# Performance work log

Measured on AMD Instinct MI355X. Metric: run time of the kernel, lower is better.

## Reference

```python
import jax, jax.numpy as jnp
import numpy as np

T, B, F = 160, 640, 40
HID, PROJ, LAYERS = 768, 256, 3


def lstm_proj_layer(x, Wk, b, Wp, reverse=False):
    # x: [T, B, in]; Wk: [in+PROJ, 4*HID]; b: [4*HID]; Wp: [HID, PROJ]
    nb = x.shape[1]
    c0 = jnp.zeros((nb, HID), x.dtype)
    h0 = jnp.zeros((nb, PROJ), x.dtype)

    def step(carry, xt):
        c, h = carry
        z = jnp.concatenate([xt, h], axis=-1) @ Wk + b
        i, j, f, o = jnp.split(z, 4, axis=-1)  # TF LSTMCell gate order i,j,f,o
        c = jax.nn.sigmoid(f + 1.0) * c + jax.nn.sigmoid(i) * jnp.tanh(j)  # forget_bias=1.0
        h = (jax.nn.sigmoid(o) * jnp.tanh(c)) @ Wp  # projection
        return (c, h), h

    _, ys = jax.lax.scan(step, (c0, h0), x, reverse=reverse)
    return ys  # [T, B, PROJ], time-aligned with input even when reverse=True


def _run_stack(x, params, reverse):
    for (Wk, b, Wp) in params:
        x = lstm_proj_layer(x, Wk, b, Wp, reverse=reverse)
    return x


def setup_inputs() -> dict:
    key = jax.random.key(0)
    keys = jax.random.split(key, 1 + 6 * LAYERS)
    inp = {"batch": jax.random.normal(keys[0], (T, B, F), dtype=jnp.float32)}
    ki = 1
    for d in ("fw", "bw"):
        for l in range(LAYERS):
            in_dim = F if l == 0 else PROJ
            inp[f"Wk_{d}{l}"] = jax.random.normal(keys[ki], (in_dim + PROJ, 4 * HID), dtype=jnp.float32) * 0.05
            inp[f"b_{d}{l}"] = jnp.zeros((4 * HID,), dtype=jnp.float32)
            inp[f"Wp_{d}{l}"] = jax.random.normal(keys[ki + 1], (HID, PROJ), dtype=jnp.float32) * 0.05
            ki += 2
    return inp


def reference(batch,
              Wk_fw0, b_fw0, Wp_fw0, Wk_fw1, b_fw1, Wp_fw1, Wk_fw2, b_fw2, Wp_fw2,
              Wk_bw0, b_bw0, Wp_bw0, Wk_bw1, b_bw1, Wp_bw1, Wk_bw2, b_bw2, Wp_bw2):
    fw_params = [(Wk_fw0, b_fw0, Wp_fw0), (Wk_fw1, b_fw1, Wp_fw1), (Wk_fw2, b_fw2, Wp_fw2)]
    bw_params = [(Wk_bw0, b_bw0, Wp_bw0), (Wk_bw1, b_bw1, Wp_bw1), (Wk_bw2, b_bw2, Wp_bw2)]
    out_fw = _run_stack(batch, fw_params, reverse=False)
    out_bw = _run_stack(batch, bw_params, reverse=True)
    outputs = jnp.concatenate([out_fw, out_bw], axis=2)  # [T, B, 2*PROJ]
    embedded = (outputs[0] + outputs[-1]) / 2.0
    # tf.nn.l2_normalize semantics
    embedded = embedded * jax.lax.rsqrt(jnp.maximum(jnp.sum(embedded * embedded, axis=-1, keepdims=True), 1e-12))
    return embedded
```

## Files before the change

### kernel.cpp

```cpp
#include <hip/hip_runtime.h>


typedef _Float16 h8 __attribute__((ext_vector_type(8)));
typedef float f4 __attribute__((ext_vector_type(4)));

#define T_STEPS 160
#define NB 640
#define HID 768
#define PROJ 256
#define NGATE 3072

__device__ __forceinline__ float sigm(float x) { return 1.0f / (1.0f + __expf(-x)); }
__device__ __forceinline__ float tanh_fast(float x) { return 2.0f / (1.0f + __expf(-2.0f * x)) - 1.0f; }

struct GateArgs {
  const _Float16* A0[6];
  const _Float16* A1[6];
  const _Float16* Bw[6];
  const float*    bias[6];
  float*          cst[6];
  _Float16*       g[6];
  int w0[6];
  int lda0[6];
  int K[6];
  int act[6];
};

struct ProjArgs {
  const _Float16* G[6];
  const _Float16* Wp[6];
  _Float16* out[6];
  _Float16* out2[6];
  int act[6];
};

__global__ __launch_bounds__(512) void gate_step(GateArgs args) {
  const int z = blockIdx.z;
  if (!args.act[z]) return;

  __shared__ __align__(16) char sm[36864];
  _Float16 (*As)[72] = (_Float16(*)[72])sm;
  _Float16 (*Bs)[72] = (_Float16(*)[72])(sm + 18432);
  float (*zs)[65] = (float(*)[65])sm;

  const _Float16* A0 = args.A0[z];
  const _Float16* A1 = args.A1[z];
  const _Float16* Bw = args.Bw[z];
  const int w0 = args.w0[z], lda0 = args.lda0[z], K = args.K[z];
  const int n0 = blockIdx.x * 128;
  const int m0 = blockIdx.y * 128;
  const int tid = threadIdx.x;
  const int lane = tid & 63;
  const int wv = tid >> 6;
  const int wm = (wv & 3) * 32;
  const int wn = (wv >> 2) * 64;

  f4 acc[2][4] = {};

  const int lr = tid >> 3;
  const int lkg = (tid & 7) * 8;

  for (int k0 = 0; k0 < K; k0 += 64) {
    const int gk = k0 + lkg;
    h8 av0, av1;
    if (gk < w0) {
      av0 = *(const h8*)(A0 + (size_t)(m0 + lr) * lda0 + gk);
      av1 = *(const h8*)(A0 + (size_t)(m0 + lr + 64) * lda0 + gk);
    } else {
      av0 = *(const h8*)(A1 + (size_t)(m0 + lr) * 256 + (gk - w0));
      av1 = *(const h8*)(A1 + (size_t)(m0 + lr + 64) * 256 + (gk - w0));
    }
    h8 bv0 = *(const h8*)(Bw + (size_t)(n0 + lr) * K + gk);
    h8 bv1 = *(const h8*)(Bw + (size_t)(n0 + lr + 64) * K + gk);
    __syncthreads();
    *(h8*)&As[lr][lkg] = av0;
    *(h8*)&As[lr + 64][lkg] = av1;
    *(h8*)&Bs[lr][lkg] = bv0;
    *(h8*)&Bs[lr + 64][lkg] = bv1;
    __syncthreads();
#pragma unroll
    for (int kk = 0; kk < 2; ++kk) {
      const int kq = ((lane >> 4) * 8) + kk * 32;
      h8 af[2], bf[4];
#pragma unroll
      for (int i = 0; i < 2; ++i)
        af[i] = *(const h8*)&As[wm + (lane & 15) + 16 * i][kq];
#pragma unroll
      for (int j = 0; j < 4; ++j)
        bf[j] = *(const h8*)&Bs[wn + (lane & 15) + 16 * j][kq];
#pragma unroll
      for (int i = 0; i < 2; ++i)
#pragma unroll
        for (int j = 0; j < 4; ++j)
          acc[i][j] = __builtin_amdgcn_mfma_f32_16x16x32_f16(af[i], bf[j], acc[i][j], 0, 0, 0);
    }
  }

  const float* bias = args.bias[z];
  float* cstate = args.cst[z];
  _Float16* gout = args.g[z];
#pragma unroll
  for (int p = 0; p < 2; ++p) {
    __syncthreads();
    if ((wv >> 2) == p) {
#pragma unroll
      for (int mi = 0; mi < 2; ++mi)
#pragma unroll
        for (int ni = 0; ni < 4; ++ni)
#pragma unroll
          for (int r = 0; r < 4; ++r) {
            int row = wm + mi * 16 + ((lane >> 4) << 2) + r;
            int col = ni * 16 + (lane & 15);
            zs[row][col] = acc[mi][ni][r];
          }
    }
    __syncthreads();
    const int u0 = (n0 + p * 64) >> 2;
#pragma unroll
    for (int it = 0; it < 4; ++it) {
      int item = it * 512 + tid;
      int row = item >> 4;
      int u = item & 15;
      float zi = zs[row][4 * u + 0] + bias[0 * HID + u0 + u];
      float zj = zs[row][4 * u + 1] + bias[1 * HID + u0 + u];
      float zf = zs[row][4 * u + 2] + bias[2 * HID + u0 + u];
      float zo = zs[row][4 * u + 3] + bias[3 * HID + u0 + u];
      size_t co = (size_t)(m0 + row) * HID + u0 + u;
      float cold = cstate[co];
      float cnew = sigm(zf + 1.0f) * cold + sigm(zi) * tanh_fast(zj);
      float g = sigm(zo) * tanh_fast(cnew);
      cstate[co] = cnew;
      gout[co] = (_Float16)g;
    }
  }
}

__global__ __launch_bounds__(256) void proj_step(ProjArgs args) {
  const int z = blockIdx.z;
  if (!args.act[z]) return;

  __shared__ __align__(16) _Float16 As[64][72];
  __shared__ __align__(16) _Float16 Bs[64][72];

  const _Float16* A = args.G[z];
  const _Float16* B = args.Wp[z];
  const int n0 = blockIdx.x * 64;
  const int m0 = blockIdx.y * 64;
  const int tid = threadIdx.x;
  const int lane = tid & 63;
  const int wv = tid >> 6;
  const int wm = (wv & 1) * 32;
  const int wn = (wv >> 1) * 32;

  f4 acc[2][2] = {};
  const int lr = tid >> 3;
  const int lkg = (tid & 7) * 8;

  for (int k0 = 0; k0 < HID; k0 += 64) {
    const int gk = k0 + lkg;
    h8 av0 = *(const h8*)(A + (size_t)(m0 + lr) * HID + gk);
    h8 av1 = *(const h8*)(A + (size_t)(m0 + lr + 32) * HID + gk);
    h8 bv0 = *(const h8*)(B + (size_t)(n0 + lr) * HID + gk);
    h8 bv1 = *(const h8*)(B + (size_t)(n0 + lr + 32) * HID + gk);
    __syncthreads();
    *(h8*)&As[lr][lkg] = av0;
    *(h8*)&As[lr + 32][lkg] = av1;
    *(h8*)&Bs[lr][lkg] = bv0;
    *(h8*)&Bs[lr + 32][lkg] = bv1;
    __syncthreads();
    const int mr = wm + (lane & 15);
    const int nr = wn + (lane & 15);
#pragma unroll
    for (int kk = 0; kk < 2; ++kk) {
      const int kq = ((lane >> 4) * 8) + kk * 32;
      h8 a0 = *(const h8*)&As[mr][kq];
      h8 a1 = *(const h8*)&As[mr + 16][kq];
      h8 b0 = *(const h8*)&Bs[nr][kq];
      h8 b1 = *(const h8*)&Bs[nr + 16][kq];
      acc[0][0] = __builtin_amdgcn_mfma_f32_16x16x32_f16(a0, b0, acc[0][0], 0, 0, 0);
      acc[0][1] = __builtin_amdgcn_mfma_f32_16x16x32_f16(a0, b1, acc[0][1], 0, 0, 0);
      acc[1][0] = __builtin_amdgcn_mfma_f32_16x16x32_f16(a1, b0, acc[1][0], 0, 0, 0);
      acc[1][1] = __builtin_amdgcn_mfma_f32_16x16x32_f16(a1, b1, acc[1][1], 0, 0, 0);
    }
  }

  _Float16* outp = args.out[z];
  _Float16* out2 = args.out2[z];
#pragma unroll
  for (int mi = 0; mi < 2; ++mi)
#pragma unroll
    for (int ni = 0; ni < 2; ++ni)
#pragma unroll
      for (int r = 0; r < 4; ++r) {
        int row = wm + mi * 16 + ((lane >> 4) << 2) + r;
        int col = wn + ni * 16 + (lane & 15);
        _Float16 v = (_Float16)acc[mi][ni][r];
        size_t o = (size_t)(m0 + row) * PROJ + (n0 + col);
        outp[o] = v;
        if (out2) out2[o] = v;
      }
}

__global__ void convX(const float* __restrict__ X, _Float16* __restrict__ X16, size_t total) {
  size_t i = (size_t)blockIdx.x * 256 + threadIdx.x;
  if (i >= total) return;
  int p = (int)(i & 63);
  size_t tb = i >> 6;
  float v = (p < 40) ? X[tb * 40 + p] : 0.0f;
  X16[i] = (_Float16)v;
}

__global__ void conv_wk(const float* __restrict__ Wk, _Float16* __restrict__ out,
                        int mode, int Kpad, size_t total) {
  size_t i = (size_t)blockIdx.x * 256 + threadIdx.x;
  if (i >= total) return;
  int k = (int)(i % Kpad);
  int n = (int)(i / Kpad);
  int u = n >> 2, g = n & 3;
  int col = g * HID + u;
  float v;
  if (mode == 0) {
    if (k < 40)      v = Wk[(size_t)k * NGATE + col];
    else if (k < 64) v = 0.0f;
    else             v = Wk[(size_t)(k - 24) * NGATE + col];
  } else {
    v = Wk[(size_t)k * NGATE + col];
  }
  out[i] = (_Float16)v;
}

__global__ void conv_wp(const float* __restrict__ Wp, _Float16* __restrict__ out, size_t total) {
  size_t i = (size_t)blockIdx.x * 256 + threadIdx.x;
  if (i >= total) return;
  int k = (int)(i % HID);
  int c = (int)(i / HID);
  out[i] = (_Float16)Wp[(size_t)k * PROJ + c];
}

__global__ __launch_bounds__(256) void readout(const _Float16* __restrict__ E, float* __restrict__ out) {
  const size_t SL = (size_t)NB * PROJ;
  int b = blockIdx.x, tid = threadIdx.x;
  float v[2];
  float ss = 0.0f;
#pragma unroll
  for (int i = 0; i < 2; ++i) {
    int j = tid + i * 256;
    int d = j >> 8, c = j & 255;
    const _Float16* base = E + (size_t)d * 2 * SL;
    float a = (float)base[(size_t)b * PROJ + c];
    float zv = (float)base[SL + (size_t)b * PROJ + c];
    v[i] = 0.5f * (a + zv);
    ss += v[i] * v[i];
  }
#pragma unroll
  for (int off = 32; off; off >>= 1) ss += __shfl_down(ss, off);
  __shared__ float ps[4];
  if ((tid & 63) == 0) ps[tid >> 6] = ss;
  __syncthreads();
  float tot = ps[0] + ps[1] + ps[2] + ps[3];
  float nrm = rsqrtf(fmaxf(tot, 1e-12f));
  out[(size_t)b * 512 + tid] = v[0] * nrm;
  out[(size_t)b * 512 + tid + 256] = v[1] * nrm;
}

extern "C" void kernel_launch(void* const* d_in, const int* in_sizes, int n_in,
                              void* d_out, int out_size, void* d_ws, size_t ws_size,
                              hipStream_t stream) {
  (void)in_sizes; (void)n_in; (void)out_size; (void)ws_size;
  const float* X = (const float*)d_in[0];
  const float* Wk[2][3]; const float* Bi[2][3]; const float* Wp[2][3];
  for (int d = 0; d < 2; ++d)
    for (int l = 0; l < 3; ++l) {
      int base = 1 + d * 9 + l * 3;
      Wk[d][l] = (const float*)d_in[base];
      Bi[d][l] = (const float*)d_in[base + 1];
      Wp[d][l] = (const float*)d_in[base + 2];
    }

  char* ws = (char*)d_ws;
  size_t off = 0;
  auto alloc = [&](size_t bytes) -> void* {
    void* p = ws + off;
    off += (bytes + 255) & ~(size_t)255;
    return p;
  };

  const size_t SL = (size_t)NB * PROJ;

  _Float16* X16 = (_Float16*)alloc((size_t)T_STEPS * NB * 64 * 2);
  _Float16* WkT[2][3];
  for (int d = 0; d < 2; ++d)
    for (int l = 0; l < 3; ++l)
      WkT[d][l] = (_Float16*)alloc((size_t)NGATE * (l == 0 ? 320 : 512) * 2);
  _Float16* WpT[2][3];
  for (int d = 0; d < 2; ++d)
    for (int l = 0; l < 3; ++l)
      WpT[d][l] = (_Float16*)alloc((size_t)PROJ * HID * 2);
  _Float16* Hbuf = (_Float16*)alloc(6UL * 4 * SL * 2);
  float* cst = (float*)alloc(6UL * NB * HID * 4);
  _Float16* gbuf = (_Float16*)alloc(6UL * NB * HID * 2);
  _Float16* embed = (_Float16*)alloc(4UL * SL * 2);

  auto Hslot = [&](int l, int d, int slot) -> _Float16* {
    return Hbuf + (((size_t)(l * 2 + d) * 4) + slot) * SL;
  };

  {
    size_t tot = (size_t)T_STEPS * NB * 64;
    convX<<<dim3((unsigned)((tot + 255) / 256)), 256, 0, stream>>>(X, X16, tot);
  }
  for (int d = 0; d < 2; ++d)
    for (int l = 0; l < 3; ++l) {
      int Kpad = (l == 0) ? 320 : 512;
      size_t tot = (size_t)NGATE * Kpad;
      conv_wk<<<dim3((unsigned)((tot + 255) / 256)), 256, 0, stream>>>(
          Wk[d][l], WkT[d][l], (l == 0) ? 0 : 1, Kpad, tot);
      size_t totp = (size_t)PROJ * HID;
      conv_wp<<<dim3((unsigned)((totp + 255) / 256)), 256, 0, stream>>>(Wp[d][l], WpT[d][l], totp);
    }
  hipMemsetAsync(Hbuf, 0, 6UL * 4 * SL * 2, stream);
  hipMemsetAsync(cst, 0, 6UL * NB * HID * 4, stream);

  for (int s = 0; s <= 161; ++s) {
    GateArgs ga{};
    ProjArgs pa{};
    for (int l = 0; l < 3; ++l)
      for (int d = 0; d < 2; ++d) {
        int z = l * 2 + d;
        int t = s - l;
        if (t < 0 || t > 159) { ga.act[z] = 0; pa.act[z] = 0; continue; }
        int tt = (d == 0) ? t : 159 - t;
        ga.act[z] = 1; pa.act[z] = 1;
        if (l == 0) {
          ga.A0[z] = X16 + (size_t)tt * NB * 64;
          ga.w0[z] = 64; ga.lda0[z] = 64; ga.K[z] = 320;
        } else {
          ga.A0[z] = Hslot(l - 1, d, (tt + 1) & 3);
          ga.w0[z] = 256; ga.lda0[z] = 256; ga.K[z] = 512;
        }
        int rdslot = (d == 0) ? (tt & 3) : ((tt + 2) & 3);
        ga.A1[z] = Hslot(l, d, rdslot);
        ga.Bw[z] = WkT[d][l];
        ga.bias[z] = Bi[d][l];
        ga.cst[z] = cst + (size_t)z * NB * HID;
        ga.g[z] = gbuf + (size_t)z * NB * HID;

        pa.G[z] = gbuf + (size_t)z * NB * HID;
        pa.Wp[z] = WpT[d][l];
        pa.out[z] = Hslot(l, d, (tt + 1) & 3);
        pa.out2[z] = nullptr;
        if (l == 2 && (tt == 0 || tt == 159))
          pa.out2[z] = embed + ((size_t)d * 2 + (tt == 0 ? 0 : 1)) * SL;
      }
    gate_step<<<dim3(24, 5, 6), 512, 0, stream>>>(ga);
    proj_step<<<dim3(4, 10, 6), 256, 0, stream>>>(pa);
  }

  readout<<<dim3(NB), 256, 0, stream>>>(embed, (float*)d_out);
}
```

Measured before the change: 6.107 ms.

## Fuse gate and projection kernels into one launch with per-row-tile atomic counters

Merges the per-timestep gate and projection kernels into a single launch of 780 blocks. The first 720 blocks compute the gate GEMM and cell update, then bump a per-(layer, row-tile) counter. The last 60 blocks spin until all 24 gate tiles for their row block have finished, then run the projection with larger 128x128 tiles. This removes one kernel launch per step and lets projection work start as soon as its rows are ready. It relies on the projection blocks being scheduled after, or alongside, the gate blocks they wait on, so it carries a spin-wait deadlock risk if residency is insufficient.

```diff
diff --git a/kernel.cpp b/kernel.cpp
--- a/kernel.cpp
+++ b/kernel.cpp
@@ -13,7 +13,7 @@
 __device__ __forceinline__ float sigm(float x) { return 1.0f / (1.0f + __expf(-x)); }
 __device__ __forceinline__ float tanh_fast(float x) { return 2.0f / (1.0f + __expf(-2.0f * x)) - 1.0f; }
 
-struct GateArgs {
+struct FArgs {
   const _Float16* A0[6];
   const _Float16* A1[6];
   const _Float16* Bw[6];
@@ -21,184 +21,191 @@
   float*          cst[6];
   _Float16*       g[6];
   int w0[6];
-  int lda0[6];
   int K[6];
   int act[6];
+  const _Float16* Wp[6];
+  _Float16* hout[6];
+  _Float16* emb[6];
+  int* cnt;
 };
 
-struct ProjArgs {
-  const _Float16* G[6];
-  const _Float16* Wp[6];
-  _Float16* out[6];
-  _Float16* out2[6];
-  int act[6];
-};
-
-__global__ __launch_bounds__(512) void gate_step(GateArgs args) {
-  const int z = blockIdx.z;
-  if (!args.act[z]) return;
-
+__global__ __launch_bounds__(512) void fused_step(FArgs args) {
   __shared__ __align__(16) char sm[36864];
   _Float16 (*As)[72] = (_Float16(*)[72])sm;
   _Float16 (*Bs)[72] = (_Float16(*)[72])(sm + 18432);
   float (*zs)[65] = (float(*)[65])sm;
 
-  const _Float16* A0 = args.A0[z];
-  const _Float16* A1 = args.A1[z];
-  const _Float16* Bw = args.Bw[z];
-  const int w0 = args.w0[z], lda0 = args.lda0[z], K = args.K[z];
-  const int n0 = blockIdx.x * 128;
-  const int m0 = blockIdx.y * 128;
   const int tid = threadIdx.x;
   const int lane = tid & 63;
   const int wv = tid >> 6;
-  const int wm = (wv & 3) * 32;
-  const int wn = (wv >> 2) * 64;
-
-  f4 acc[2][4] = {};
-
   const int lr = tid >> 3;
   const int lkg = (tid & 7) * 8;
 
-  for (int k0 = 0; k0 < K; k0 += 64) {
-    const int gk = k0 + lkg;
-    h8 av0, av1;
-    if (gk < w0) {
-      av0 = *(const h8*)(A0 + (size_t)(m0 + lr) * lda0 + gk);
-      av1 = *(const h8*)(A0 + (size_t)(m0 + lr + 64) * lda0 + gk);
-    } else {
-      av0 = *(const h8*)(A1 + (size_t)(m0 + lr) * 256 + (gk - w0));
-      av1 = *(const h8*)(A1 + (size_t)(m0 + lr + 64) * 256 + (gk - w0));
-    }
-    h8 bv0 = *(const h8*)(Bw + (size_t)(n0 + lr) * K + gk);
-    h8 bv1 = *(const h8*)(Bw + (size_t)(n0 + lr + 64) * K + gk);
+  if (blockIdx.x < 720) {
+    const int tile = blockIdx.x;
+    const int z = tile / 120;
+    const int rem = tile - z * 120;
+    if (!args.act[z]) return;
+    const int n0 = (rem % 24) * 128;
+    const int by = rem / 24;
+    const int m0 = by * 128;
+
+    const _Float16* A0 = args.A0[z];
+    const _Float16* A1 = args.A1[z];
+    const _Float16* Bw = args.Bw[z];
+    const int w0 = args.w0[z], K = args.K[z];
+    const int wm = (wv & 3) * 32;
+    const int wn = (wv >> 2) * 64;
+
+    f4 acc[2][4] = {};
+
+    for (int k0 = 0; k0 < K; k0 += 64) {
+      const int gk = k0 + lkg;
+      h8 av0, av1;
+      if (gk < w0) {
+        av0 = *(const h8*)(A0 + (size_t)(m0 + lr) * w0 + gk);
+        av1 = *(const h8*)(A0 + (size_t)(m0 + lr + 64) * w0 + gk);
+      } else {
+        av0 = *(const h8*)(A1 + (size_t)(m0 + lr) * 256 + (gk - w0));
+        av1 = *(const h8*)(A1 + (size_t)(m0 + lr + 64) * 256 + (gk - w0));
+      }
+      h8 bv0 = *(const h8*)(Bw + (size_t)(n0 + lr) * K + gk);
+      h8 bv1 = *(const h8*)(Bw + (size_t)(n0 + lr + 64) * K + gk);
+      __syncthreads();
+      *(h8*)&As[lr][lkg] = av0;
+      *(h8*)&As[lr + 64][lkg] = av1;
+      *(h8*)&Bs[lr][lkg] = bv0;
+      *(h8*)&Bs[lr + 64][lkg] = bv1;
+      __syncthreads();
+#pragma unroll
+      for (int kk = 0; kk < 2; ++kk) {
+        const int kq = ((lane >> 4) * 8) + kk * 32;
+        h8 af[2], bf[4];
+#pragma unroll
+        for (int i = 0; i < 2; ++i)
+          af[i] = *(const h8*)&As[wm + (lane & 15) + 16 * i][kq];
+#pragma unroll
+        for (int j = 0; j < 4; ++j)
+          bf[j] = *(const h8*)&Bs[wn + (lane & 15) + 16 * j][kq];
+#pragma unroll
+        for (int i = 0; i < 2; ++i)
+#pragma unroll
+          for (int j = 0; j < 4; ++j)
+            acc[i][j] = __builtin_amdgcn_mfma_f32_16x16x32_f16(af[i], bf[j], acc[i][j], 0, 0, 0);
+      }
+    }
+
+    const float* bias = args.bias[z];
+    float* cstate = args.cst[z];
+    _Float16* gout = args.g[z];
+#pragma unroll
+    for (int p = 0; p < 2; ++p) {
+      __syncthreads();
+      if ((wv >> 2) == p) {
+#pragma unroll
+        for (int mi = 0; mi < 2; ++mi)
+#pragma unroll
+          for (int ni = 0; ni < 4; ++ni)
+#pragma unroll
+            for (int r = 0; r < 4; ++r) {
+              int row = wm + mi * 16 + ((lane >> 4) << 2) + r;
+              int col = ni * 16 + (lane & 15);
+              zs[row][col] = acc[mi][ni][r];
+            }
+      }
+      __syncthreads();
+      const int u0 = (n0 + p * 64) >> 2;
+#pragma unroll
+      for (int it = 0; it < 4; ++it) {
+        int item = it * 512 + tid;
+        int row = item >> 4;
+        int u = item & 15;
+        float zi = zs[row][4 * u + 0] + bias[0 * HID + u0 + u];
+        float zj = zs[row][4 * u + 1] + bias[1 * HID + u0 + u];
+        float zf = zs[row][4 * u + 2] + bias[2 * HID + u0 + u];
+        float zo = zs[row][4 * u + 3] + bias[3 * HID + u0 + u];
+        size_t co = (size_t)(m0 + row) * HID + u0 + u;
+        float cold = cstate[co];
+        float cnew = sigm(zf + 1.0f) * cold + sigm(zi) * tanh_fast(zj);
+        float g = sigm(zo) * tanh_fast(cnew);
+        cstate[co] = cnew;
+        gout[co] = (_Float16)g;
+      }
+    }
+
     __syncthreads();
-    *(h8*)&As[lr][lkg] = av0;
-    *(h8*)&As[lr + 64][lkg] = av1;
-    *(h8*)&Bs[lr][lkg] = bv0;
-    *(h8*)&Bs[lr + 64][lkg] = bv1;
+    if (tid == 0) {
+      __threadfence();
+      atomicAdd(args.cnt + z * 5 + by, 1);
+    }
+  } else {
+    const int p = blockIdx.x - 720;
+    const int z = p / 10;
+    const int rem = p - z * 10;
+    if (!args.act[z]) return;
+    const int n0 = (rem & 1) * 128;
+    const int by = rem >> 1;
+    const int m0 = by * 128;
+
+    if (tid == 0) {
+      int* c = args.cnt + z * 5 + by;
+      while (atomicOr(c, 0) < 24) __builtin_amdgcn_s_sleep(2);
+      __threadfence();
+    }
     __syncthreads();
-#pragma unroll
-    for (int kk = 0; kk < 2; ++kk) {
-      const int kq = ((lane >> 4) * 8) + kk * 32;
-      h8 af[2], bf[4];
-#pragma unroll
-      for (int i = 0; i < 2; ++i)
-        af[i] = *(const h8*)&As[wm + (lane & 15) + 16 * i][kq];
-#pragma unroll
-      for (int j = 0; j < 4; ++j)
-        bf[j] = *(const h8*)&Bs[wn + (lane & 15) + 16 * j][kq];
-#pragma unroll
-      for (int i = 0; i < 2; ++i)
+
+    const _Float16* A = args.g[z];
+    const _Float16* B = args.Wp[z];
+    const int wm = (wv & 3) * 32;
+    const int wn = (wv >> 2) * 64;
+
+    f4 acc[2][4] = {};
+    for (int k0 = 0; k0 < HID; k0 += 64) {
+      const int gk = k0 + lkg;
+      h8 av0 = *(const h8*)(A + (size_t)(m0 + lr) * HID + gk);
+      h8 av1 = *(const h8*)(A + (size_t)(m0 + lr + 64) * HID + gk);
+      h8 bv0 = *(const h8*)(B + (size_t)(n0 + lr) * HID + gk);
+      h8 bv1 = *(const h8*)(B + (size_t)(n0 + lr + 64) * HID + gk);
+      __syncthreads();
+      *(h8*)&As[lr][lkg] = av0;
+      *(h8*)&As[lr + 64][lkg] = av1;
+      *(h8*)&Bs[lr][lkg] = bv0;
+      *(h8*)&Bs[lr + 64][lkg] = bv1;
+      __syncthreads();
+#pragma unroll
+      for (int kk = 0; kk < 2; ++kk) {
+        const int kq = ((lane >> 4) * 8) + kk * 32;
+        h8 af[2], bf[4];
+#pragma unroll
+        for (int i = 0; i < 2; ++i)
+          af[i] = *(const h8*)&As[wm + (lane & 15) + 16 * i][kq];
 #pragma unroll
         for (int j = 0; j < 4; ++j)
-          acc[i][j] = __builtin_amdgcn_mfma_f32_16x16x32_f16(af[i], bf[j], acc[i][j], 0, 0, 0);
-    }
-  }
-
-  const float* bias = args.bias[z];
-  float* cstate = args.cst[z];
-  _Float16* gout = args.g[z];
-#pragma unroll
-  for (int p = 0; p < 2; ++p) {
-    __syncthreads();
-    if ((wv >> 2) == p) {
-#pragma unroll
-      for (int mi = 0; mi < 2; ++mi)
-#pragma unroll
-        for (int ni = 0; ni < 4; ++ni)
-#pragma unroll
-          for (int r = 0; r < 4; ++r) {
-            int row = wm + mi * 16 + ((lane >> 4) << 2) + r;
-            int col = ni * 16 + (lane & 15);
-            zs[row][col] = acc[mi][ni][r];
-          }
-    }
-    __syncthreads();
-    const int u0 = (n0 + p * 64) >> 2;
-#pragma unroll
-    for (int it = 0; it < 4; ++it) {
-      int item = it * 512 + tid;
-      int row = item >> 4;
-      int u = item & 15;
-      float zi = zs[row][4 * u + 0] + bias[0 * HID + u0 + u];
-      float zj = zs[row][4 * u + 1] + bias[1 * HID + u0 + u];
-      float zf = zs[row][4 * u + 2] + bias[2 * HID + u0 + u];
-      float zo = zs[row][4 * u + 3] + bias[3 * HID + u0 + u];
-      size_t co = (size_t)(m0 + row) * HID + u0 + u;
-      float cold = cstate[co];
-      float cnew = sigm(zf + 1.0f) * cold + sigm(zi) * tanh_fast(zj);
-      float g = sigm(zo) * tanh_fast(cnew);
-      cstate[co] = cnew;
-      gout[co] = (_Float16)g;
-    }
-  }
-}
-
-__global__ __launch_bounds__(256) void proj_step(ProjArgs args) {
-  const int z = blockIdx.z;
-  if (!args.act[z]) return;
-
-  __shared__ __align__(16) _Float16 As[64][72];
-  __shared__ __align__(16) _Float16 Bs[64][72];
-
-  const _Float16* A = args.G[z];
-  const _Float16* B = args.Wp[z];
-  const int n0 = blockIdx.x * 64;
-  const int m0 = blockIdx.y * 64;
-  const int tid = threadIdx.x;
-  const int lane = tid & 63;
-  const int wv = tid >> 6;
-  const int wm = (wv & 1) * 32;
-  const int wn = (wv >> 1) * 32;
-
-  f4 acc[2][2] = {};
-  const int lr = tid >> 3;
-  const int lkg = (tid & 7) * 8;
-
-  for (int k0 = 0; k0 < HID; k0 += 64) {
-    const int gk = k0 + lkg;
-    h8 av0 = *(const h8*)(A + (size_t)(m0 + lr) * HID + gk);
-    h8 av1 = *(const h8*)(A + (size_t)(m0 + lr + 32) * HID + gk);
-    h8 bv0 = *(const h8*)(B + (size_t)(n0 + lr) * HID + gk);
-    h8 bv1 = *(const h8*)(B + (size_t)(n0 + lr + 32) * HID + gk);
-    __syncthreads();
-    *(h8*)&As[lr][lkg] = av0;
-    *(h8*)&As[lr + 32][lkg] = av1;
-    *(h8*)&Bs[lr][lkg] = bv0;
-    *(h8*)&Bs[lr + 32][lkg] = bv1;
-    __syncthreads();
-    const int mr = wm + (lane & 15);
-    const int nr = wn + (lane & 15);
-#pragma unroll
-    for (int kk = 0; kk < 2; ++kk) {
-      const int kq = ((lane >> 4) * 8) + kk * 32;
-      h8 a0 = *(const h8*)&As[mr][kq];
-      h8 a1 = *(const h8*)&As[mr + 16][kq];
-      h8 b0 = *(const h8*)&Bs[nr][kq];
-      h8 b1 = *(const h8*)&Bs[nr + 16][kq];
-      acc[0][0] = __builtin_amdgcn_mfma_f32_16x16x32_f16(a0, b0, acc[0][0], 0, 0, 0);
-      acc[0][1] = __builtin_amdgcn_mfma_f32_16x16x32_f16(a0, b1, acc[0][1], 0, 0, 0);
-      acc[1][0] = __builtin_amdgcn_mfma_f32_16x16x32_f16(a1, b0, acc[1][0], 0, 0, 0);
-      acc[1][1] = __builtin_amdgcn_mfma_f32_16x16x32_f16(a1, b1, acc[1][1], 0, 0, 0);
-    }
-  }
-
-  _Float16* outp = args.out[z];
-  _Float16* out2 = args.out2[z];
-#pragma unroll
-  for (int mi = 0; mi < 2; ++mi)
-#pragma unroll
-    for (int ni = 0; ni < 2; ++ni)
-#pragma unroll
-      for (int r = 0; r < 4; ++r) {
-        int row = wm + mi * 16 + ((lane >> 4) << 2) + r;
-        int col = wn + ni * 16 + (lane & 15);
-        _Float16 v = (_Float16)acc[mi][ni][r];
-        size_t o = (size_t)(m0 + row) * PROJ + (n0 + col);
-        outp[o] = v;
-        if (out2) out2[o] = v;
-      }
+          bf[j] = *(const h8*)&Bs[wn + (lane & 15) + 16 * j][kq];
+#pragma unroll
+        for (int i = 0; i < 2; ++i)
+#pragma unroll
+          for (int j = 0; j < 4; ++j)
+            acc[i][j] = __builtin_amdgcn_mfma_f32_16x16x32_f16(af[i], bf[j], acc[i][j], 0, 0, 0);
+      }
+    }
+
+    _Float16* outp = args.hout[z];
+    _Float16* out2 = args.emb[z];
+#pragma unroll
+    for (int mi = 0; mi < 2; ++mi)
+#pragma unroll
+      for (int ni = 0; ni < 4; ++ni)
+#pragma unroll
+        for (int r = 0; r < 4; ++r) {
+          int row = wm + mi * 16 + ((lane >> 4) << 2) + r;
+          int col = wn + ni * 16 + (lane & 15);
+          _Float16 v = (_Float16)acc[mi][ni][r];
+          size_t o = (size_t)(m0 + row) * PROJ + (n0 + col);
+          outp[o] = v;
+          if (out2) out2[o] = v;
+        }
+  }
 }
 
 __global__ void convX(const float* __restrict__ X, _Float16* __restrict__ X16, size_t total) {
@@ -300,6 +307,7 @@
   float* cst = (float*)alloc(6UL * NB * HID * 4);
   _Float16* gbuf = (_Float16*)alloc(6UL * NB * HID * 2);
   _Float16* embed = (_Float16*)alloc(4UL * SL * 2);
+  int* cntbuf = (int*)alloc(162UL * 30 * 4);
 
   auto Hslot = [&](int l, int d, int slot) -> _Float16* {
     return Hbuf + (((size_t)(l * 2 + d) * 4) + slot) * SL;
@@ -320,40 +328,39 @@
     }
   hipMemsetAsync(Hbuf, 0, 6UL * 4 * SL * 2, stream);
   hipMemsetAsync(cst, 0, 6UL * NB * HID * 4, stream);
+  hipMemsetAsync(cntbuf, 0, 162UL * 30 * 4, stream);
 
   for (int s = 0; s <= 161; ++s) {
-    GateArgs ga{};
-    ProjArgs pa{};
+    FArgs fa{};
+    fa.cnt = cntbuf + (size_t)s * 30;
     for (int l = 0; l < 3; ++l)
       for (int d = 0; d < 2; ++d) {
         int z = l * 2 + d;
         int t = s - l;
-        if (t < 0 || t > 159) { ga.act[z] = 0; pa.act[z] = 0; continue; }
+        if (t < 0 || t > 159) { fa.act[z] = 0; continue; }
         int tt = (d == 0) ? t : 159 - t;
-        ga.act[z] = 1; pa.act[z] = 1;
+        fa.act[z] = 1;
         if (l == 0) {
-          ga.A0[z] = X16 + (size_t)tt * NB * 64;
-          ga.w0[z] = 64; ga.lda0[z] = 64; ga.K[z] = 320;
+          fa.A0[z] = X16 + (size_t)tt * NB * 64;
+          fa.w0[z] = 64; fa.K[z] = 320;
         } else {
-          ga.A0[z] = Hslot(l - 1, d, (tt + 1) & 3);
-          ga.w0[z] = 256; ga.lda0[z] = 256; ga.K[z] = 512;
+          fa.A0[z] = Hslot(l - 1, d, (tt + 1) & 3);
+          fa.w0[z] = 256; fa.K[z] = 512;
         }
         int rdslot = (d == 0) ? (tt & 3) : ((tt + 2) & 3);
-        ga.A1[z] = Hslot(l, d, rdslot);
-        ga.Bw[z] = WkT[d][l];
-        ga.bias[z] = Bi[d][l];
-        ga.cst[z] = cst + (size_t)z * NB * HID;
-        ga.g[z] = gbuf + (size_t)z * NB * HID;
-
-        pa.G[z] = gbuf + (size_t)z * NB * HID;
-        pa.Wp[z] = WpT[d][l];
-        pa.out[z] = Hslot(l, d, (tt + 1) & 3);
-        pa.out2[z] = nullptr;
+        fa.A1[z] = Hslot(l, d, rdslot);
+        fa.Bw[z] = WkT[d][l];
+        fa.bias[z] = Bi[d][l];
+        fa.cst[z] = cst + (size_t)z * NB * HID;
+        fa.g[z] = gbuf + (size_t)z * NB * HID;
+
+        fa.Wp[z] = WpT[d][l];
+        fa.hout[z] = Hslot(l, d, (tt + 1) & 3);
+        fa.emb[z] = nullptr;
         if (l == 2 && (tt == 0 || tt == 159))
-          pa.out2[z] = embed + ((size_t)d * 2 + (tt == 0 ? 0 : 1)) * SL;
-      }
-    gate_step<<<dim3(24, 5, 6), 512, 0, stream>>>(ga);
-    proj_step<<<dim3(4, 10, 6), 256, 0, stream>>>(pa);
+          fa.emb[z] = embed + ((size_t)d * 2 + (tt == 0 ? 0 : 1)) * SL;
+      }
+    fused_step<<<dim3(780), 512, 0, stream>>>(fa);
   }
 
   readout<<<dim3(NB), 256, 0, stream>>>(embed, (float*)d_out);
```

After: 12.44 ms. +103.7%, slower.
